# Kernel tuning notes

Measured on AMD Instinct MI355X. Metric: run time of the kernel, lower is better.

Reference implementation:

```python
import jax, jax.numpy as jnp
from jax import lax
import numpy as np

# larq-style ste_sign: forward sign (with sign(0)=+1), straight-through grad clipped to |x|<=1
@jax.custom_vjp
def ste_sign(x):
    return jnp.where(x >= 0, 1.0, -1.0).astype(x.dtype)

def _ste_fwd(x):
    return ste_sign(x), x

def _ste_bwd(x, g):
    return (g * (jnp.abs(x) <= 1.0).astype(g.dtype),)

ste_sign.defvjp(_ste_fwd, _ste_bwd)


def setup_inputs() -> dict:
    key = jax.random.key(0)
    k1, k2 = jax.random.split(key)
    B, H, Wd, Cin = 16, 256, 256, 32
    M, kh, kw, Cout = 4, 3, 3, 32
    x = jax.random.normal(k1, (B, H, Wd, Cin), dtype=jnp.float32)
    W = jax.random.normal(k2, (M, kh, kw, Cin, Cout), dtype=jnp.float32)
    b = jnp.zeros((M, Cout), dtype=jnp.float32)
    return {"x": x, "W": W, "b": b}


def reference(x, W, b):
    # Multibin: sum_{m} QuantConv2D_m(x).  Each branch binarizes the SAME input,
    # so sum of convs == one conv with the sum of the binarized kernels (fused).
    xq = ste_sign(x)                 # [B,H,W,Cin], values in {-1,+1}
    wq = ste_sign(W)                 # [M,kh,kw,Cin,Cout]
    w_sum = wq.sum(axis=0)           # [kh,kw,Cin,Cout]
    y = lax.conv_general_dilated(
        xq, w_sum,
        window_strides=(1, 1),
        padding="SAME",
        dimension_numbers=("NHWC", "HWIO", "NHWC"),
    )
    return y + b.sum(axis=0)         # [B,H,W,Cout]
```

## Files before the change

### kernel.cpp

```cpp
#include <hip/hip_runtime.h>


#define RH      8
#define NSTAGE  34
#define PITCHB  48
#define SLOTB   (NSTAGE * PITCHB)

typedef __attribute__((ext_vector_type(4)))  int i32x4;
typedef __attribute__((ext_vector_type(16))) int i32x16;

__device__ __forceinline__ unsigned int pack4(float4 v, bool ok) {
    if (!ok) return 0u;
    unsigned r = (v.x >= 0.0f) ? 0x01u : 0xFFu;
    r |= ((v.y >= 0.0f) ? 0x01u : 0xFFu) << 8;
    r |= ((v.z >= 0.0f) ? 0x01u : 0xFFu) << 16;
    r |= ((v.w >= 0.0f) ? 0x01u : 0xFFu) << 24;
    return r;
}

__global__ void prep_kernel(const float* __restrict__ W, const float* __restrict__ bias,
                            signed char* __restrict__ wsT, float* __restrict__ bsum) {
    int t = blockIdx.x * 256 + threadIdx.x;
    if (t < 9216) {
        int k   = t >> 5;
        int co  = t & 31;
        int tap = k >> 5;
        int ci  = k & 31;
        float s = 0.0f;
        #pragma unroll
        for (int m = 0; m < 4; ++m) {
            float w = W[(m * 9 + tap) * 1024 + ci * 32 + co];
            s += (w >= 0.0f) ? 1.0f : -1.0f;
        }
        wsT[co * 288 + k] = (signed char)(int)s;
    }
    if (t < 32) {
        float s = 0.0f;
        #pragma unroll
        for (int m = 0; m < 4; ++m) s += bias[m * 32 + t];
        bsum[t] = s;
    }
}

__global__ __launch_bounds__(64, 4) void conv_kernel(const float* __restrict__ x,
                                                     const signed char* __restrict__ wsT,
                                                     const float* __restrict__ bsum,
                                                     float* __restrict__ out) {
    __shared__ __align__(16) unsigned char lds[4 * SLOTB];

    const int lane = threadIdx.x;
    const int lrow = lane & 31;
    const int lk   = lane >> 5;

    const int bs   = blockIdx.x;
    const int c0   = (bs & 7) * 32;
    const int r0   = ((bs >> 3) & 31) * RH;
    const int bimg = bs >> 8;

    i32x4 bfrag[9];
    #pragma unroll
    for (int t = 0; t < 9; ++t)
        bfrag[t] = *(const i32x4*)(wsT + lrow * 288 + t * 32 + lk * 16);
    const float bsv = bsum[lrow];

    #pragma unroll
    for (int pre = 0; pre < 3; ++pre) {
        const int absrow = r0 - 1 + pre;
        const bool rowok = (absrow >= 0) && (absrow < 256);
        const float* rowp = x + (long)((bimg * 256 + absrow) * 256) * 32;
        unsigned char* dst = lds + pre * SLOTB;
        #pragma unroll
        for (int p = 0; p < 3; ++p) {
            int f = lane + p * 64;
            int pix = f >> 2, ch = f & 3;
            if (pix < NSTAGE) {
                int col = c0 - 1 + pix;
                bool ok = rowok && (col >= 0) && (col < 256);
                const float4* pp = (const float4*)(rowp + (long)col * 32 + ch * 8);
                float4 v0 = ok ? pp[0] : make_float4(0.f, 0.f, 0.f, 0.f);
                float4 v1 = ok ? pp[1] : make_float4(0.f, 0.f, 0.f, 0.f);
                *(uint2*)(dst + pix * PITCHB + ch * 8) =
                    make_uint2(pack4(v0, ok), pack4(v1, ok));
            }
        }
    }

    const int a_off = lrow * PITCHB + lk * 16;

    #pragma unroll 4
    for (int i = 0; i < RH; ++i) {
        const int r = r0 + i;
        const bool do_pf = (i < RH - 1);
        const int absrow = r + 2;
        const bool rowok = do_pf && (absrow < 256);
        const float* rowp = x + (long)((bimg * 256 + absrow) * 256) * 32;

        float4 v0[3], v1[3];
        #pragma unroll
        for (int p = 0; p < 3; ++p) {
            int f = lane + p * 64;
            int pix = f >> 2, ch = f & 3;
            int col = c0 - 1 + pix;
            bool ok = rowok && (pix < NSTAGE) && (col >= 0) && (col < 256);
            const float4* pp = (const float4*)(rowp + (long)col * 32 + ch * 8);
            v0[p] = ok ? pp[0] : make_float4(0.f, 0.f, 0.f, 0.f);
            v1[p] = ok ? pp[1] : make_float4(0.f, 0.f, 0.f, 0.f);
        }

        i32x16 acc = {};
        #pragma unroll
        for (int dh = 0; dh < 3; ++dh) {
            const unsigned char* sb = lds + ((i + dh) & 3) * SLOTB + a_off;
            #pragma unroll
            for (int dw = 0; dw < 3; ++dw) {
                i32x4 a = *(const i32x4*)(sb + dw * PITCHB);
                acc = __builtin_amdgcn_mfma_i32_32x32x32_i8(a, bfrag[dh * 3 + dw],
                                                            acc, 0, 0, 0);
            }
        }

        float* op = out + ((long)((bimg * 256 + r) * 256 + c0)) * 32 + lrow;
        #pragma unroll
        for (int reg = 0; reg < 16; ++reg) {
            int pr = (reg & 3) + 8 * (reg >> 2) + 4 * lk;
            __builtin_nontemporal_store((float)acc[reg] + bsv, op + pr * 32);
        }

        if (do_pf) {
            unsigned char* dst = lds + ((i + 3) & 3) * SLOTB;
            #pragma unroll
            for (int p = 0; p < 3; ++p) {
                int f = lane + p * 64;
                int pix = f >> 2, ch = f & 3;
                if (pix < NSTAGE) {
                    int col = c0 - 1 + pix;
                    bool ok = (absrow < 256) && (col >= 0) && (col < 256);
                    *(uint2*)(dst + pix * PITCHB + ch * 8) =
                        make_uint2(pack4(v0[p], ok), pack4(v1[p], ok));
                }
            }
        }
    }
}

extern "C" void kernel_launch(void* const* d_in, const int* in_sizes, int n_in,
                              void* d_out, int out_size, void* d_ws, size_t ws_size,
                              hipStream_t stream) {
    const float* x    = (const float*)d_in[0];
    const float* W    = (const float*)d_in[1];
    const float* bias = (const float*)d_in[2];
    float* out = (float*)d_out;

    signed char* wsT = (signed char*)d_ws;
    float* bsum = (float*)((char*)d_ws + 9216);

    prep_kernel<<<36, 256, 0, stream>>>(W, bias, wsT, bsum);
    conv_kernel<<<4096, 64, 0, stream>>>(x, wsT, bsum, out);
}
```

Baseline: 248.9 us.

## Deepen row prefetch to two rows ahead with double-buffered registers

Global loads for input rows are now issued two iterations ahead and held in double-buffered register arrays, so each load has roughly a full extra iteration of MFMA and store work to hide behind. The three prologue rows are all issued before any is packed, and the per-lane index and bounds math is hoisted out of the loop. The main loop is also fully unrolled. This costs more VGPRs (six extra float4 arrays), which could hurt occupancy under the 4-wave launch bound.

```diff
diff --git a/kernel.cpp b/kernel.cpp
--- a/kernel.cpp
+++ b/kernel.cpp
@@ -42,6 +42,35 @@
     }
 }
 
+#define ISSUE(ABSROW, V0, V1)                                                   \
+    do {                                                                        \
+        const int absrow_ = (ABSROW);                                           \
+        const bool rowok_ = (absrow_ >= 0) && (absrow_ < 256);                  \
+        const float* rowp_ = x + (long)((bimg * 256 + absrow_) * 256) * 32;     \
+        _Pragma("unroll")                                                       \
+        for (int p = 0; p < 3; ++p) {                                           \
+            bool ok = rowok_ && cok[p];                                         \
+            const float4* pp = (const float4*)(rowp_ + ldoff[p]);               \
+            V0[p] = ok ? pp[0] : make_float4(0.f, 0.f, 0.f, 0.f);               \
+            V1[p] = ok ? pp[1] : make_float4(0.f, 0.f, 0.f, 0.f);               \
+        }                                                                       \
+    } while (0)
+
+#define COMMIT(ABSROW, SL, V0, V1)                                              \
+    do {                                                                        \
+        const int absrow_ = (ABSROW);                                           \
+        const bool rowok_ = (absrow_ >= 0) && (absrow_ < 256);                  \
+        unsigned char* dst_ = lds + (SL) * SLOTB;                               \
+        _Pragma("unroll")                                                       \
+        for (int p = 0; p < 3; ++p) {                                           \
+            if (pvalid[p]) {                                                    \
+                bool ok = rowok_ && cok[p];                                     \
+                *(uint2*)(dst_ + pix[p] * PITCHB + ch[p] * 8) =                 \
+                    make_uint2(pack4(V0[p], ok), pack4(V1[p], ok));             \
+            }                                                                   \
+        }                                                                       \
+    } while (0)
+
 __global__ __launch_bounds__(64, 4) void conv_kernel(const float* __restrict__ x,
                                                      const signed char* __restrict__ wsT,
                                                      const float* __restrict__ bsum,
@@ -57,55 +86,41 @@
     const int r0   = ((bs >> 3) & 31) * RH;
     const int bimg = bs >> 8;
 
+    int pix[3], ch[3]; bool pvalid[3], cok[3]; long ldoff[3];
+    #pragma unroll
+    for (int p = 0; p < 3; ++p) {
+        int f = lane + p * 64;
+        pix[p] = f >> 2; ch[p] = f & 3;
+        pvalid[p] = (pix[p] < NSTAGE);
+        int col = c0 - 1 + pix[p];
+        cok[p] = pvalid[p] && (col >= 0) && (col < 256);
+        ldoff[p] = (long)col * 32 + ch[p] * 8;
+    }
+
+    float4 pa0[3], pa1[3], pb0[3], pb1[3], pc0[3], pc1[3];
+    ISSUE(r0 - 1, pa0, pa1);
+    ISSUE(r0,     pb0, pb1);
+    ISSUE(r0 + 1, pc0, pc1);
+    COMMIT(r0 - 1, 0, pa0, pa1);
+    COMMIT(r0,     1, pb0, pb1);
+    COMMIT(r0 + 1, 2, pc0, pc1);
+
     i32x4 bfrag[9];
     #pragma unroll
     for (int t = 0; t < 9; ++t)
         bfrag[t] = *(const i32x4*)(wsT + lrow * 288 + t * 32 + lk * 16);
     const float bsv = bsum[lrow];
 
-    #pragma unroll
-    for (int pre = 0; pre < 3; ++pre) {
-        const int absrow = r0 - 1 + pre;
-        const bool rowok = (absrow >= 0) && (absrow < 256);
-        const float* rowp = x + (long)((bimg * 256 + absrow) * 256) * 32;
-        unsigned char* dst = lds + pre * SLOTB;
-        #pragma unroll
-        for (int p = 0; p < 3; ++p) {
-            int f = lane + p * 64;
-            int pix = f >> 2, ch = f & 3;
-            if (pix < NSTAGE) {
-                int col = c0 - 1 + pix;
-                bool ok = rowok && (col >= 0) && (col < 256);
-                const float4* pp = (const float4*)(rowp + (long)col * 32 + ch * 8);
-                float4 v0 = ok ? pp[0] : make_float4(0.f, 0.f, 0.f, 0.f);
-                float4 v1 = ok ? pp[1] : make_float4(0.f, 0.f, 0.f, 0.f);
-                *(uint2*)(dst + pix * PITCHB + ch * 8) =
-                    make_uint2(pack4(v0, ok), pack4(v1, ok));
-            }
-        }
-    }
+    float4 b0[2][3], b1[2][3];
+    ISSUE(r0 + 2, b0[0], b1[0]);
 
     const int a_off = lrow * PITCHB + lk * 16;
 
-    #pragma unroll 4
+    #pragma unroll
     for (int i = 0; i < RH; ++i) {
-        const int r = r0 + i;
-        const bool do_pf = (i < RH - 1);
-        const int absrow = r + 2;
-        const bool rowok = do_pf && (absrow < 256);
-        const float* rowp = x + (long)((bimg * 256 + absrow) * 256) * 32;
+        const int cur = i & 1, nxt = cur ^ 1;
 
-        float4 v0[3], v1[3];
-        #pragma unroll
-        for (int p = 0; p < 3; ++p) {
-            int f = lane + p * 64;
-            int pix = f >> 2, ch = f & 3;
-            int col = c0 - 1 + pix;
-            bool ok = rowok && (pix < NSTAGE) && (col >= 0) && (col < 256);
-            const float4* pp = (const float4*)(rowp + (long)col * 32 + ch * 8);
-            v0[p] = ok ? pp[0] : make_float4(0.f, 0.f, 0.f, 0.f);
-            v1[p] = ok ? pp[1] : make_float4(0.f, 0.f, 0.f, 0.f);
-        }
+        if (i <= RH - 3) ISSUE(r0 + i + 3, b0[nxt], b1[nxt]);
 
         i32x16 acc = {};
         #pragma unroll
@@ -119,27 +134,14 @@
             }
         }
 
-        float* op = out + ((long)((bimg * 256 + r) * 256 + c0)) * 32 + lrow;
+        float* op = out + ((long)((bimg * 256 + (r0 + i)) * 256 + c0)) * 32 + lrow;
         #pragma unroll
         for (int reg = 0; reg < 16; ++reg) {
             int pr = (reg & 3) + 8 * (reg >> 2) + 4 * lk;
             __builtin_nontemporal_store((float)acc[reg] + bsv, op + pr * 32);
         }
 
-        if (do_pf) {
-            unsigned char* dst = lds + ((i + 3) & 3) * SLOTB;
-            #pragma unroll
-            for (int p = 0; p < 3; ++p) {
-                int f = lane + p * 64;
-                int pix = f >> 2, ch = f & 3;
-                if (pix < NSTAGE) {
-                    int col = c0 - 1 + pix;
-                    bool ok = (absrow < 256) && (col >= 0) && (col < 256);
-                    *(uint2*)(dst + pix * PITCHB + ch * 8) =
-                        make_uint2(pack4(v0[p], ok), pack4(v1[p], ok));
-                }
-            }
-        }
+        if (i <= RH - 2) COMMIT(r0 + i + 2, (i + 3) & 3, b0[cur], b1[cur]);
     }
 }
 
```

New measurement: 257.2 us. +3.3%, slower.
